# Kernel tuning notes

Measured on AMD Instinct MI355X. Metric: run time of the kernel, lower is better.

The kernel has to match this reference:

```python
import jax, jax.numpy as jnp
import numpy as np
from jax import lax

T, B, H, W, C = 256, 64, 7, 7, 3
HID = 128
HIST = 16
EMB = 128  # conv output channels; 7->4->2->1 spatial, so embed dim = 128


def setup_inputs() -> dict:
    key = jax.random.key(0)
    ks = jax.random.split(key, 16)
    s = 0.05
    inp = {
        "inputs": jax.random.normal(ks[0], (T, B, H, W, C), jnp.float32),
        "done": jax.random.bernoulli(ks[1], 0.05, (T, B)),
        # conv feature extractor (OIHW)
        "conv1_w": jax.random.normal(ks[2], (32, 3, 3, 3), jnp.float32) * s,
        "conv1_b": jnp.zeros((32,), jnp.float32),
        "conv2_w": jax.random.normal(ks[3], (32, 32, 3, 3), jnp.float32) * s,
        "conv2_b": jnp.zeros((32,), jnp.float32),
        "conv3_w": jax.random.normal(ks[4], (EMB, 32, 3, 3), jnp.float32) * s,
        "conv3_b": jnp.zeros((EMB,), jnp.float32),
        # readin: Linear(128 -> HID)
        "readin_w": jax.random.normal(ks[5], (HID, EMB), jnp.float32) * s,
        "readin_b": jnp.zeros((HID,), jnp.float32),
        # LSTMCell(HID, HID)
        "w_ih": jax.random.normal(ks[6], (4 * HID, HID), jnp.float32) * s,
        "w_hh": jax.random.normal(ks[7], (4 * HID, HID), jnp.float32) * s,
        "b_ih": jnp.zeros((4 * HID,), jnp.float32),
        "b_hh": jnp.zeros((4 * HID,), jnp.float32),
        # readout: Linear(HID -> 128)
        "readout_w": jax.random.normal(ks[8], (EMB, HID), jnp.float32) * s,
        "readout_b": jnp.zeros((EMB,), jnp.float32),
    }
    return inp


def _conv(x, w, b):
    # stride 2, padding 1, NCHW / OIHW
    y = lax.conv_general_dilated(x, w, (2, 2), [(1, 1), (1, 1)],
                                 dimension_numbers=("NCHW", "OIHW", "NCHW"))
    return y + b[None, :, None, None]


def _pad_unfold(x, hist):
    # x: [T, B, C] -> [hist, T*B, C]; contexts[h, t] = padded_x[t + h]
    xp = jnp.pad(x, ((hist - 1, 0), (0, 0), (0, 0)))
    ctx = jnp.stack([xp[h:h + x.shape[0]] for h in range(hist)], axis=0)
    return ctx.reshape(hist, x.shape[0] * x.shape[1], x.shape[2])


def reference(inputs, done, conv1_w, conv1_b, conv2_w, conv2_b, conv3_w, conv3_b,
              readin_w, readin_b, w_ih, w_hh, b_ih, b_hh, readout_w, readout_b):
    # --- embed (MinigridStateEmbeddingNet) ---
    x = inputs.reshape(T * B, H, W, C).astype(jnp.float32)
    x = jnp.transpose(x, (0, 3, 2, 1))  # torch transpose(1,3): [TB, C, W, H]
    x = jax.nn.elu(_conv(x, conv1_w, conv1_b))
    x = jax.nn.elu(_conv(x, conv2_w, conv2_b))
    x = jax.nn.elu(_conv(x, conv3_w, conv3_b))
    x = x.reshape(T, B, -1)  # [T, B, 128]

    # --- readin ---
    x = x @ readin_w.T + readin_b  # [T, B, HID]

    # --- pad_unfold over time history ---
    ctx = _pad_unfold(x, HIST)                               # [HIST, T*B, HID]
    d = done[:, :, None]                                     # [T, B, 1] bool
    dctx = _pad_unfold(d, HIST)                              # [HIST, T*B, 1]

    # --- run_sequence: LSTM scan with done-masked resets ---
    def lstm_step(xt, h, c):
        gates = xt @ w_ih.T + b_ih + h @ w_hh.T + b_hh
        i, f, g, o = jnp.split(gates, 4, axis=-1)
        c2 = jax.nn.sigmoid(f) * c + jax.nn.sigmoid(i) * jnp.tanh(g)
        h2 = jax.nn.sigmoid(o) * jnp.tanh(c2)
        return h2, c2

    zeros = jnp.zeros((T * B, HID), jnp.float32)
    h1, c1 = lstm_step(ctx[0], zeros, zeros)

    def step(carry, xd):
        h, c = carry
        xt, dt = xd
        h = jnp.where(dt, 0.0, h)
        c = jnp.where(dt, 0.0, c)
        h, c = lstm_step(xt, h, c)
        return (h, c), h

    _, hs = lax.scan(step, (h1, c1), (ctx[1:], dctx[1:]))
    outputs = jnp.concatenate([h1[None], hs], axis=0)        # [HIST, T*B, HID]

    # --- readout, take last history step ---
    out = outputs @ readout_w.T + readout_b                  # [HIST, T*B, 128]
    out = out.reshape(HIST, T, B, EMB)[-1]                   # [T, B, 128]
    return out
```

## Files before the change

kernel.cpp:

```cpp
#include <hip/hip_runtime.h>

typedef _Float16 half8 __attribute__((ext_vector_type(8)));
typedef _Float16 half4 __attribute__((ext_vector_type(4)));
typedef float f32x4 __attribute__((ext_vector_type(4)));

__device__ __forceinline__ float eluf(float x)   { return x > 0.f ? x : __expf(x) - 1.f; }
__device__ __forceinline__ float sigf(float x) {
  return __builtin_amdgcn_rcpf(1.f + __expf(-x));
}
__device__ __forceinline__ float tanhff(float x) {
  return 1.f - 2.f * __builtin_amdgcn_rcpf(__expf(2.f * x) + 1.f);
}

__device__ __forceinline__ half8 cvt8(const float* __restrict__ p) {
  f32x4 v0 = *(const f32x4*)p;
  f32x4 v1 = *(const f32x4*)(p + 4);
  half8 r;
  r[0] = (_Float16)v0[0]; r[1] = (_Float16)v0[1]; r[2] = (_Float16)v0[2]; r[3] = (_Float16)v0[3];
  r[4] = (_Float16)v1[0]; r[5] = (_Float16)v1[1]; r[6] = (_Float16)v1[2]; r[7] = (_Float16)v1[3];
  return r;
}
#define MFMA(a, b, c) __builtin_amdgcn_mfma_f32_16x16x32_f16(a, b, c, 0, 0, 0)

__global__ __launch_bounds__(256) void k_done(const unsigned char* __restrict__ raw,
                                              unsigned long long* __restrict__ dmask) {
  __shared__ int f0, f1;
  if (threadIdx.x == 0) { f0 = 0; f1 = 0; }
  __syncthreads();
  int l0 = 0, l1 = 0;
  for (int i = threadIdx.x; i < 16384; i += 256)
    if (raw[i]) { if (i & 3) l0 = 1; else l1 = 1; }
  if (l0) atomicOr(&f0, 1);
  if (l1) atomicOr(&f1, 1);
  __syncthreads();
  int mode = (f0 && f1) ? 0 : (f1 ? 1 : (f0 ? 2 : 0));
  const int t = blockIdx.x;
  if (threadIdx.x < 64) {
    int i = t * 64 + threadIdx.x;
    bool v;
    if (mode == 0)      v = raw[i] != 0;
    else if (mode == 1) v = ((const int*)raw)[i] != 0;
    else                v = (((const float*)raw)[i] != 0.f);
    unsigned long long m = __ballot(v);
    if (threadIdx.x == 0) dmask[t] = m;
  }
}

__global__ __launch_bounds__(512, 4) void k_conv(
    const float* __restrict__ inp,
    const float* __restrict__ c1w, const float* __restrict__ c1b,
    const float* __restrict__ c2w, const float* __restrict__ c2b,
    const float* __restrict__ c3w, const float* __restrict__ c3b,
    const float* __restrict__ riw, const float* __restrict__ rib,
    const float* __restrict__ wih, const float* __restrict__ bih,
    const float* __restrict__ bhh,
    _Float16* __restrict__ xgh)
{
  extern __shared__ char L[];
  unsigned*  LUT32 = (unsigned*)L;
  _Float16*  ic1   = (_Float16*)(L + 128);
  _Float16*  a1t   = (_Float16*)(L + 16512);
  _Float16*  a2    = (_Float16*)(L + 53632);
  _Float16*  c2wL  = (_Float16*)(L + 61824);
  _Float16*  ft    = (_Float16*)(L + 128);
  _Float16*  yb    = (_Float16*)(L + 8320);

  const int tid  = threadIdx.x;
  const int lane = tid & 63;
  const int wv   = tid >> 6;
  const int lr   = lane & 15;
  const int lg   = lane >> 4;
  const int t    = blockIdx.x >> 1;
  const int bh   = blockIdx.x & 1;

  const int ntl  = wv & 1;
  const int mq   = wv >> 1;
  const int o1   = ntl * 16 + lr;

  if (tid < 32) {
    unsigned v = 0xFFFFFFFFu;
    if (tid < 27) { int c = tid / 9, r9 = tid % 9; v = (unsigned)(c | ((r9 / 3) << 8) | ((r9 % 3) << 16)); }
    LUT32[tid] = v;
  }

  if (tid < 128) {
    const int o = tid >> 2, lg2 = tid & 3;
    const float* src = c2w + o * 288 + lg2 * 72;
    #pragma unroll 4
    for (int j = 0; j < 72; ++j) {
      int i = lg2 * 8 + j / 9, tap = j % 9;
      c2wL[(o * 9 + tap) * 32 + i] = (_Float16)src[j];
    }
  }

  half8 B1;
  #pragma unroll
  for (int e = 0; e < 8; ++e) {
    int k = lg * 8 + e;
    B1[e] = (_Float16)((k < 27) ? c1w[o1 * 27 + k] : 0.f);
  }
  const float b1o = c1b[o1];
  const float b2o = c2b[o1];

  for (int ch = 0; ch < 2; ++ch) {
    __syncthreads();
    for (int i = tid; i < 18560 / 2; i += 512) ((unsigned*)a1t)[i] = 0u;
    {
      const size_t n0 = (size_t)(t * 64 + bh * 32 + ch * 16) * 147;
      #pragma unroll 4
      for (int j = 0; j < 16; ++j) {
        int e = tid + j * 512;
        int row = e >> 5, k = e & 31;
        int s = row >> 4, pos = row & 15;
        int p = pos >> 2, q = pos & 3;
        unsigned lut = LUT32[k];
        float v = 0.f;
        if (lut != 0xFFFFFFFFu) {
          int c = lut & 0xFF, dp = (lut >> 8) & 0xFF, dq = (lut >> 16) & 0xFF;
          int pp = 2 * p + dp - 1, qq = 2 * q + dq - 1;
          if ((unsigned)pp < 7u && (unsigned)qq < 7u)
            v = inp[n0 + s * 147 + qq * 21 + pp * 3 + c];
        }
        ic1[row * 32 + (k ^ ((row & 3) << 3))] = (_Float16)v;
      }
    }
    __syncthreads();
    #pragma unroll
    for (int mi = 0; mi < 4; ++mi) {
      const int mtile = mq * 4 + mi;
      const int rowA  = mtile * 16 + lr;
      half8 a = *(const half8*)(ic1 + rowA * 32 + ((lg * 8) ^ ((rowA & 3) << 3)));
      f32x4 acc; acc[0] = b1o; acc[1] = b1o; acc[2] = b1o; acc[3] = b1o;
      acc = MFMA(a, B1, acc);
      #pragma unroll
      for (int r = 0; r < 4; ++r) {
        int m1 = mtile * 16 + lg * 4 + r;
        int s = m1 >> 4, pos = m1 & 15;
        int p = pos >> 2, q = pos & 3;
        int xy = (p + 1) * 6 + (q + 1);
        a1t[s * 1160 + xy * 32 + (o1 ^ ((xy & 3) << 3))] = (_Float16)eluf(acc[r]);
      }
    }
    __syncthreads();
    {
      f32x4 acc; acc[0] = b2o; acc[1] = b2o; acc[2] = b2o; acc[3] = b2o;
      const int rowm = mq * 16 + lr;
      const int s2 = rowm >> 2, pos2 = rowm & 3;
      const int p2 = pos2 >> 1, q2 = pos2 & 1;
      #pragma unroll
      for (int tap = 0; tap < 9; ++tap) {
        const int dp = tap / 3, dq = tap % 3;
        const int xy2 = (2 * p2 + dp) * 6 + (2 * q2 + dq);
        half8 a  = *(const half8*)(a1t + s2 * 1160 + xy2 * 32 + ((lg * 8) ^ ((xy2 & 3) << 3)));
        half8 b2 = *(const half8*)(c2wL + (o1 * 9 + tap) * 32 + lg * 8);
        acc = MFMA(a, b2, acc);
      }
      #pragma unroll
      for (int r = 0; r < 4; ++r) {
        int m = mq * 16 + lg * 4 + r;
        int s2w = m >> 2, pos = m & 3;
        int arow = ch * 16 + s2w;
        int col = o1 * 4 + pos;
        a2[arow * 128 + (col ^ ((arow & 7) << 3))] = (_Float16)eluf(acc[r]);
      }
    }
  }
  __syncthreads();

  {
    half8 B3[4];
    #pragma unroll
    for (int kt = 0; kt < 4; ++kt) {
      half8 b;
      #pragma unroll
      for (int e = 0; e < 8; ++e) {
        int k = kt * 32 + lg * 8 + e;
        int i = k >> 2, pos = k & 3;
        int widx = 4 + (pos >> 1) * 3 + (pos & 1);
        b[e] = (_Float16)c3w[(wv * 16 + lr) * 288 + i * 9 + widx];
      }
      B3[kt] = b;
    }
    float bb = c3b[wv * 16 + lr];
    #pragma unroll
    for (int mt = 0; mt < 2; ++mt) {
      f32x4 acc; acc[0] = bb; acc[1] = bb; acc[2] = bb; acc[3] = bb;
      const int row = mt * 16 + lr;
      #pragma unroll
      for (int kt = 0; kt < 4; ++kt) {
        half8 a = *(const half8*)(a2 + row * 128 + ((kt * 32 + lg * 8) ^ ((row & 7) << 3)));
        acc = MFMA(a, B3[kt], acc);
      }
      #pragma unroll
      for (int r = 0; r < 4; ++r) {
        int m = mt * 16 + lg * 4 + r;
        ft[m * 128 + ((wv * 16 + lr) ^ ((m & 7) << 3))] = (_Float16)eluf(acc[r]);
      }
    }
  }
  __syncthreads();

  {
    half8 R1[4];
    #pragma unroll
    for (int kt = 0; kt < 4; ++kt)
      R1[kt] = cvt8(riw + (wv * 16 + lr) * 128 + kt * 32 + lg * 8);
    float bb = rib[wv * 16 + lr];
    #pragma unroll
    for (int mt = 0; mt < 2; ++mt) {
      f32x4 acc; acc[0] = bb; acc[1] = bb; acc[2] = bb; acc[3] = bb;
      const int row = mt * 16 + lr;
      #pragma unroll
      for (int kt = 0; kt < 4; ++kt) {
        half8 a = *(const half8*)(ft + row * 128 + ((kt * 32 + lg * 8) ^ ((row & 7) << 3)));
        acc = MFMA(a, R1[kt], acc);
      }
      #pragma unroll
      for (int r = 0; r < 4; ++r) {
        int m = mt * 16 + lg * 4 + r;
        yb[m * 128 + ((wv * 16 + lr) ^ ((m & 7) << 3))] = (_Float16)acc[r];
      }
    }
  }
  __syncthreads();

  {
    #pragma unroll
    for (int mt = 0; mt < 2; ++mt) {
      const int row = mt * 16 + lr;
      half8 a[4];
      #pragma unroll
      for (int kt = 0; kt < 4; ++kt)
        a[kt] = *(const half8*)(yb + row * 128 + ((kt * 32 + lg * 8) ^ ((row & 7) << 3)));
      #pragma unroll
      for (int ty = 0; ty < 4; ++ty) {
        int g = ty * 128 + wv * 16 + lr;
        float bg = bih[g] + bhh[g];
        f32x4 acc; acc[0] = bg; acc[1] = bg; acc[2] = bg; acc[3] = bg;
        #pragma unroll
        for (int kt = 0; kt < 4; ++kt) {
          half8 w = cvt8(wih + g * 128 + kt * 32 + lg * 8);
          acc = MFMA(a[kt], w, acc);
        }
        half4 h4;
        h4[0] = (_Float16)acc[0]; h4[1] = (_Float16)acc[1];
        h4[2] = (_Float16)acc[2]; h4[3] = (_Float16)acc[3];
        *(half4*)(xgh + ((size_t)t * 512 + g) * 64 + bh * 32 + mt * 16 + lg * 4) = h4;
      }
    }
  }
}

__global__ __launch_bounds__(512, 2) void k_lstm(
    const float* __restrict__ whh, const float* __restrict__ bih,
    const float* __restrict__ bhh, const _Float16* __restrict__ xgh,
    const unsigned long long* __restrict__ dmask,
    const float* __restrict__ row_, const float* __restrict__ rob,
    float* __restrict__ out)
{
  __shared__ _Float16 H[2][32 * 128];

  const int tid  = threadIdx.x;
  const int lane = tid & 63;
  const int wv   = tid >> 6;
  const int lr   = lane & 15, lg = lane >> 4;
  const int xcd  = blockIdx.x & 7;
  const int j    = blockIdx.x >> 3;
  const int t    = (xcd << 5) + (j >> 1);
  const int bh   = j & 1;
  const int bbase = bh * 32;

  half8 Wf[4][4];
  float b0[4];
  #pragma unroll
  for (int ty = 0; ty < 4; ++ty) {
    int g = ty * 128 + wv * 16 + lr;
    b0[ty] = bih[g] + bhh[g];
    #pragma unroll
    for (int kt = 0; kt < 4; ++kt)
      Wf[kt][ty] = cvt8(whh + g * 128 + kt * 32 + lg * 8);
  }

  for (int i = tid; i < 32 * 128 / 2; i += 512) ((unsigned*)H[0])[i] = 0u;

  float cc[2][4];
  #pragma unroll
  for (int mt = 0; mt < 2; ++mt)
    #pragma unroll
    for (int r = 0; r < 4; ++r) cc[mt][r] = 0.f;

  for (int st = 0; st < 16; ++st) {
    const int ts = t + st - 15;
    _Float16* Hr = H[st & 1];
    _Float16* Hw = H[(st & 1) ^ 1];
    __syncthreads();
    const bool hasX = (ts >= 0);
    const unsigned long long wm =
        (st < 15 && ts + 1 >= 0) ? dmask[ts + 1] : 0ULL;
    const _Float16* xb = xgh + (size_t)ts * 32768 + bbase;
    #pragma unroll
    for (int mt = 0; mt < 2; ++mt) {
      const int rowA = mt * 16 + lr;
      half8 afr[4];
      #pragma unroll
      for (int kt = 0; kt < 4; ++kt)
        afr[kt] = *(const half8*)(Hr + rowA * 128 + ((kt * 32 + lg * 8) ^ ((rowA & 7) << 3)));
      f32x4 acc[4];
      if (hasX) {
        #pragma unroll
        for (int ty = 0; ty < 4; ++ty) {
          half4 p = *(const half4*)(xb + (ty * 128 + wv * 16 + lr) * 64 + mt * 16 + lg * 4);
          acc[ty][0] = (float)p[0]; acc[ty][1] = (float)p[1];
          acc[ty][2] = (float)p[2]; acc[ty][3] = (float)p[3];
        }
      } else {
        #pragma unroll
        for (int ty = 0; ty < 4; ++ty) {
          acc[ty][0] = b0[ty]; acc[ty][1] = b0[ty]; acc[ty][2] = b0[ty]; acc[ty][3] = b0[ty];
        }
      }
      __builtin_amdgcn_s_setprio(1);
      #pragma unroll
      for (int ty = 0; ty < 4; ++ty)
        #pragma unroll
        for (int kt = 0; kt < 4; ++kt)
          acc[ty] = MFMA(afr[kt], Wf[kt][ty], acc[ty]);
      __builtin_amdgcn_s_setprio(0);
      const unsigned mnib = (unsigned)(wm >> (bbase + mt * 16 + lg * 4)) & 15u;
      #pragma unroll
      for (int r = 0; r < 4; ++r) {
        const int s_ = mt * 16 + lg * 4 + r;
        const bool d = (mnib >> r) & 1u;
        float iv = sigf(acc[0][r]);
        float fv = sigf(acc[1][r]);
        float gv = tanhff(acc[2][r]);
        float ov = sigf(acc[3][r]);
        float cn = fmaf(fv, cc[mt][r], iv * gv);
        float hn = ov * tanhff(cn);
        cc[mt][r] = d ? 0.f : cn;
        Hw[s_ * 128 + ((wv * 16 + lr) ^ ((s_ & 7) << 3))] = (_Float16)(d ? 0.f : hn);
      }
    }
  }
  __syncthreads();

  half8 R[4];
  #pragma unroll
  for (int kt = 0; kt < 4; ++kt)
    R[kt] = cvt8(row_ + (wv * 16 + lr) * 128 + kt * 32 + lg * 8);
  float rb2 = rob[wv * 16 + lr];
  #pragma unroll
  for (int mt = 0; mt < 2; ++mt) {
    const int row = mt * 16 + lr;
    f32x4 acc; acc[0] = rb2; acc[1] = rb2; acc[2] = rb2; acc[3] = rb2;
    #pragma unroll
    for (int kt = 0; kt < 4; ++kt) {
      half8 a = *(const half8*)(H[0] + row * 128 + ((kt * 32 + lg * 8) ^ ((row & 7) << 3)));
      acc = MFMA(a, R[kt], acc);
    }
    #pragma unroll
    for (int r = 0; r < 4; ++r) {
      int s = mt * 16 + lg * 4 + r;
      out[(size_t)(t * 64 + bbase + s) * 128 + wv * 16 + lr] = acc[r];
    }
  }
}

extern "C" void kernel_launch(void* const* d_in, const int* in_sizes, int n_in,
                              void* d_out, int out_size, void* d_ws, size_t ws_size,
                              hipStream_t stream) {
  const float* inp = (const float*)d_in[0];
  const void*  don = d_in[1];
  const float* c1w = (const float*)d_in[2];
  const float* c1b = (const float*)d_in[3];
  const float* c2w = (const float*)d_in[4];
  const float* c2b = (const float*)d_in[5];
  const float* c3w = (const float*)d_in[6];
  const float* c3b = (const float*)d_in[7];
  const float* riw = (const float*)d_in[8];
  const float* rib = (const float*)d_in[9];
  const float* wih = (const float*)d_in[10];
  const float* whh = (const float*)d_in[11];
  const float* bih = (const float*)d_in[12];
  const float* bhh = (const float*)d_in[13];
  const float* row_ = (const float*)d_in[14];
  const float* rob = (const float*)d_in[15];

  unsigned long long* dmask = (unsigned long long*)d_ws;
  _Float16* xgh = (_Float16*)((char*)d_ws + 16384);

  (void)hipFuncSetAttribute((const void*)k_conv,
                            hipFuncAttributeMaxDynamicSharedMemorySize, 80256);

  k_done<<<256, 256, 0, stream>>>((const unsigned char*)don, dmask);
  k_conv<<<512, 512, 80256, stream>>>(inp, c1w, c1b, c2w, c2b, c3w, c3b,
                                      riw, rib, wih, bih, bhh, xgh);
  k_lstm<<<512, 512, 0, stream>>>(whh, bih, bhh, xgh, dmask, row_, rob,
                                  (float*)d_out);
}
```

Before: 208.5 us.

## Prepack W_hh to fp16 fragment layout and stream it per k-tile in LSTM

The k_done kernel now also converts W_hh to fp16 and writes it to a workspace in MFMA fragment order. k_lstm no longer keeps all 16 W_hh fragments in registers for the whole kernel. Instead it reloads four coalesced fp16 fragments per k-tile on every step and interleaves both M-tiles over each k-tile. This is meant to lower register pressure and drop the per-block fp32 to fp16 conversion, at the cost of repeated global or L2 weight reads inside the serial 16-step loop.

```diff
diff --git a/kernel.cpp b/kernel.cpp
--- a/kernel.cpp
+++ b/kernel.cpp
@@ -23,7 +23,9 @@
 #define MFMA(a, b, c) __builtin_amdgcn_mfma_f32_16x16x32_f16(a, b, c, 0, 0, 0)
 
 __global__ __launch_bounds__(256) void k_done(const unsigned char* __restrict__ raw,
-                                              unsigned long long* __restrict__ dmask) {
+                                              const float* __restrict__ whh,
+                                              unsigned long long* __restrict__ dmask,
+                                              _Float16* __restrict__ whhF) {
   __shared__ int f0, f1;
   if (threadIdx.x == 0) { f0 = 0; f1 = 0; }
   __syncthreads();
@@ -43,6 +45,13 @@
     else                v = (((const float*)raw)[i] != 0.f);
     unsigned long long m = __ballot(v);
     if (threadIdx.x == 0) dmask[t] = m;
+  }
+  {
+    int i = blockIdx.x * 256 + threadIdx.x;
+    int g = i >> 7, k = i & 127;
+    int wc = (g >> 4) & 7, lr = g & 15, ty = g >> 7;
+    int kt = k >> 5, lg = (k >> 3) & 3, e = k & 7;
+    whhF[(((wc * 4 + kt) * 4 + ty) * 64 + lg * 16 + lr) * 8 + e] = (_Float16)whh[i];
   }
 }
 
@@ -252,7 +261,7 @@
 }
 
 __global__ __launch_bounds__(512, 2) void k_lstm(
-    const float* __restrict__ whh, const float* __restrict__ bih,
+    const _Float16* __restrict__ whhF, const float* __restrict__ bih,
     const float* __restrict__ bhh, const _Float16* __restrict__ xgh,
     const unsigned long long* __restrict__ dmask,
     const float* __restrict__ row_, const float* __restrict__ rob,
@@ -270,15 +279,13 @@
   const int bh   = j & 1;
   const int bbase = bh * 32;
 
-  half8 Wf[4][4];
+  const _Float16* wbase = whhF + (size_t)wv * 8192 + lane * 8;
+
   float b0[4];
   #pragma unroll
   for (int ty = 0; ty < 4; ++ty) {
     int g = ty * 128 + wv * 16 + lr;
     b0[ty] = bih[g] + bhh[g];
-    #pragma unroll
-    for (int kt = 0; kt < 4; ++kt)
-      Wf[kt][ty] = cvt8(whh + g * 128 + kt * 32 + lg * 8);
   }
 
   for (int i = tid; i < 32 * 128 / 2; i += 512) ((unsigned*)H[0])[i] = 0u;
@@ -298,43 +305,52 @@
     const unsigned long long wm =
         (st < 15 && ts + 1 >= 0) ? dmask[ts + 1] : 0ULL;
     const _Float16* xb = xgh + (size_t)ts * 32768 + bbase;
-    #pragma unroll
-    for (int mt = 0; mt < 2; ++mt) {
-      const int rowA = mt * 16 + lr;
-      half8 afr[4];
-      #pragma unroll
-      for (int kt = 0; kt < 4; ++kt)
-        afr[kt] = *(const half8*)(Hr + rowA * 128 + ((kt * 32 + lg * 8) ^ ((rowA & 7) << 3)));
-      f32x4 acc[4];
-      if (hasX) {
+    f32x4 acc[2][4];
+    if (hasX) {
+      #pragma unroll
+      for (int mt = 0; mt < 2; ++mt)
         #pragma unroll
         for (int ty = 0; ty < 4; ++ty) {
           half4 p = *(const half4*)(xb + (ty * 128 + wv * 16 + lr) * 64 + mt * 16 + lg * 4);
-          acc[ty][0] = (float)p[0]; acc[ty][1] = (float)p[1];
-          acc[ty][2] = (float)p[2]; acc[ty][3] = (float)p[3];
+          acc[mt][ty][0] = (float)p[0]; acc[mt][ty][1] = (float)p[1];
+          acc[mt][ty][2] = (float)p[2]; acc[mt][ty][3] = (float)p[3];
         }
-      } else {
+    } else {
+      #pragma unroll
+      for (int mt = 0; mt < 2; ++mt)
         #pragma unroll
         for (int ty = 0; ty < 4; ++ty) {
-          acc[ty][0] = b0[ty]; acc[ty][1] = b0[ty]; acc[ty][2] = b0[ty]; acc[ty][3] = b0[ty];
+          acc[mt][ty][0] = b0[ty]; acc[mt][ty][1] = b0[ty];
+          acc[mt][ty][2] = b0[ty]; acc[mt][ty][3] = b0[ty];
         }
-      }
+    }
+    #pragma unroll
+    for (int kt = 0; kt < 4; ++kt) {
+      half8 wf[4];
+      #pragma unroll
+      for (int ty = 0; ty < 4; ++ty)
+        wf[ty] = *(const half8*)(wbase + (kt * 4 + ty) * 512);
+      half8 a0 = *(const half8*)(Hr + lr * 128 + ((kt * 32 + lg * 8) ^ ((lr & 7) << 3)));
+      half8 a1 = *(const half8*)(Hr + (16 + lr) * 128 + ((kt * 32 + lg * 8) ^ (((16 + lr) & 7) << 3)));
       __builtin_amdgcn_s_setprio(1);
       #pragma unroll
-      for (int ty = 0; ty < 4; ++ty)
-        #pragma unroll
-        for (int kt = 0; kt < 4; ++kt)
-          acc[ty] = MFMA(afr[kt], Wf[kt][ty], acc[ty]);
+      for (int ty = 0; ty < 4; ++ty) {
+        acc[0][ty] = MFMA(a0, wf[ty], acc[0][ty]);
+        acc[1][ty] = MFMA(a1, wf[ty], acc[1][ty]);
+      }
       __builtin_amdgcn_s_setprio(0);
+    }
+    #pragma unroll
+    for (int mt = 0; mt < 2; ++mt) {
       const unsigned mnib = (unsigned)(wm >> (bbase + mt * 16 + lg * 4)) & 15u;
       #pragma unroll
       for (int r = 0; r < 4; ++r) {
         const int s_ = mt * 16 + lg * 4 + r;
         const bool d = (mnib >> r) & 1u;
-        float iv = sigf(acc[0][r]);
-        float fv = sigf(acc[1][r]);
-        float gv = tanhff(acc[2][r]);
-        float ov = sigf(acc[3][r]);
+        float iv = sigf(acc[mt][0][r]);
+        float fv = sigf(acc[mt][1][r]);
+        float gv = tanhff(acc[mt][2][r]);
+        float ov = sigf(acc[mt][3][r]);
         float cn = fmaf(fv, cc[mt][r], iv * gv);
         float hn = ov * tanhff(cn);
         cc[mt][r] = d ? 0.f : cn;
@@ -387,14 +403,15 @@
   const float* rob = (const float*)d_in[15];
 
   unsigned long long* dmask = (unsigned long long*)d_ws;
-  _Float16* xgh = (_Float16*)((char*)d_ws + 16384);
+  _Float16* whhF = (_Float16*)((char*)d_ws + 16384);
+  _Float16* xgh  = (_Float16*)((char*)d_ws + 16384 + 131072);
 
   (void)hipFuncSetAttribute((const void*)k_conv,
                             hipFuncAttributeMaxDynamicSharedMemorySize, 80256);
 
-  k_done<<<256, 256, 0, stream>>>((const unsigned char*)don, dmask);
+  k_done<<<256, 256, 0, stream>>>((const unsigned char*)don, whh, dmask, whhF);
   k_conv<<<512, 512, 80256, stream>>>(inp, c1w, c1b, c2w, c2b, c3w, c3b,
                                       riw, rib, wih, bih, bhh, xgh);
-  k_lstm<<<512, 512, 0, stream>>>(whh, bih, bhh, xgh, dmask, row_, rob,
+  k_lstm<<<512, 512, 0, stream>>>(whhF, bih, bhh, xgh, dmask, row_, rob,
                                   (float*)d_out);
 }
```

Result: no change. 211.6 us (+1.5%).
